# Performance work log

Hardware: AMD Instinct MI355X
Metric: run time of the kernel (lower is better)

## Reference

```python
import jax, jax.numpy as jnp
import numpy as np

N = 100000  # nodes

def gcn_layer(x, W, b, src, dst, norm):
    # x: [N, Fin] -> [N, Fout]; symmetric-normalized aggregation (PyG GCNConv)
    h = x @ W                                   # linear first (no bias yet)
    msg = h[src] * norm[:, None]                # gather + edge-wise scale
    out = jax.ops.segment_sum(msg, dst, num_segments=N)  # scatter-add to targets
    return out + b

def _prep_edges(edge_index):
    # add self loops
    loops = jnp.arange(N, dtype=edge_index.dtype)
    src = jnp.concatenate([edge_index[0], loops])
    dst = jnp.concatenate([edge_index[1], loops])
    # deg computed on target nodes with unit edge weights
    deg = jax.ops.segment_sum(jnp.ones_like(dst, dtype=jnp.float32), dst, num_segments=N)
    dinv = jnp.where(deg > 0, jax.lax.rsqrt(deg), 0.0)
    norm = dinv[src] * dinv[dst]
    return src, dst, norm

def setup_inputs() -> dict:
    key = jax.random.key(0)
    ks = jax.random.split(key, 8)
    F_in, H1, H2, C = 512, 256, 64, 10
    E = 3200000
    x = jax.random.normal(ks[0], (N, F_in), dtype=jnp.float32)
    edge_index = jax.random.randint(ks[1], (2, E), 0, N, dtype=jnp.int64)
    def glorot(k, fan_in, fan_out):
        s = jnp.sqrt(6.0 / (fan_in + fan_out))
        return jax.random.uniform(k, (fan_in, fan_out), jnp.float32, -s, s)
    return {
        "x": x,
        "edge_index": edge_index,
        "W1": glorot(ks[2], F_in, H1), "b1": jnp.zeros((H1,), jnp.float32),
        "W2": glorot(ks[3], H1, H2),   "b2": jnp.zeros((H2,), jnp.float32),
        "W3": glorot(ks[4], H2, C),    "b3": jnp.zeros((C,), jnp.float32),
    }

def reference(x, edge_index, W1, b1, W2, b2, W3, b3):
    src, dst, norm = _prep_edges(edge_index)
    h = jax.nn.relu(gcn_layer(x, W1, b1, src, dst, norm))
    h = jax.nn.relu(gcn_layer(h, W2, b2, src, dst, norm))
    h = gcn_layer(h, W3, b3, src, dst, norm)
    return jax.nn.log_softmax(h, axis=1)
```

## Files before the change

### kernel.cpp

```cpp
#include <hip/hip_runtime.h>
#include <math.h>

#define NNODES 100000
#define NEDGES 3200000
#define NB 391
#define PB 512
#define CHUNK 6250

typedef __attribute__((ext_vector_type(4))) float f32x4;
typedef __attribute__((ext_vector_type(2))) float f32x2;
typedef __attribute__((ext_vector_type(8))) short bf16x8;

__device__ __forceinline__ float bf2f(ushort u) {
    union { unsigned u; float f; } v; v.u = ((unsigned)u) << 16; return v.f;
}
__device__ __forceinline__ ushort f2bf(float f) {
    union { float f; unsigned u; } v; v.f = f;
    unsigned r = v.u + 0x7FFFu + ((v.u >> 16) & 1u);
    return (ushort)(r >> 16);
}

__device__ __forceinline__ unsigned pack_bf2(float f0, float f1) {
    union { float f; unsigned u; } a, b; a.f = f0; b.f = f1;
#if __has_builtin(__builtin_amdgcn_perm)
    return __builtin_amdgcn_perm(b.u, a.u, 0x07060302u);
#else
    return (b.u & 0xFFFF0000u) | (a.u >> 16);
#endif
}

#if __has_builtin(__builtin_amdgcn_cvt_pk_fp8_f32) && __has_builtin(__builtin_amdgcn_cvt_pk_f32_fp8)
#define FP8_HW 1
#else
#define FP8_HW 0
#endif

__device__ __forceinline__ unsigned fp8enc_sw(float f) {
    union { float f; unsigned u; } v; v.f = f;
    unsigned sign = v.u >> 31;
    float a = fabsf(f);
    if (a >= 448.0f) return (sign << 7) | 0x7E;
    if (a < 0.0009765625f) return sign << 7;
    unsigned u = v.u & 0x7FFFFFFFu;
    u += 0x7FFFFu + ((u >> 20) & 1u);
    int e2 = (int)(u >> 23) - 127;
    if (e2 < -6) {
        int m = (int)(a * 512.0f + 0.5f); if (m > 7) m = 7;
        return (sign << 7) | (unsigned)m;
    }
    if (e2 > 8) return (sign << 7) | 0x7E;
    unsigned mant = (u >> 20) & 7u;
    return (sign << 7) | ((unsigned)(e2 + 7) << 3) | mant;
}
__device__ __forceinline__ float fp8dec_sw(unsigned b) {
    unsigned s = b >> 7, e = (b >> 3) & 0xF, m = b & 7;
    float v;
    if (e == 0) v = (float)m * 0.001953125f;
    else { union { unsigned u; float f; } x; x.u = ((e + 120u) << 23) | (m << 20); v = x.f; }
    return s ? -v : v;
}

__device__ __forceinline__ unsigned char f2fp8(float f) {
#if FP8_HW
    return (unsigned char)(__builtin_amdgcn_cvt_pk_fp8_f32(f, 0.f, 0, false) & 0xFF);
#else
    return (unsigned char)fp8enc_sw(f);
#endif
}
__device__ __forceinline__ void fp8x4_acc2(unsigned w, f32x2& a01, f32x2& a23) {
#if FP8_HW
    a01 += __builtin_amdgcn_cvt_pk_f32_fp8((int)w, false);
    a23 += __builtin_amdgcn_cvt_pk_f32_fp8((int)w, true);
#else
    a01[0] += fp8dec_sw(w & 0xFF); a01[1] += fp8dec_sw((w >> 8) & 0xFF);
    a23[0] += fp8dec_sw((w >> 16) & 0xFF); a23[1] += fp8dec_sw(w >> 24);
#endif
}

__global__ void bucket_hist(const int* __restrict__ dst, int e, int* __restrict__ hist) {
    __shared__ int h[NB];
    const int b = blockIdx.x, t = threadIdx.x;
    for (int j = t; j < NB; j += 256) h[j] = 0;
    __syncthreads();
    const int lo = b * CHUNK;
    int hi = lo + CHUNK; if (hi > e) hi = e;
    for (int i = lo + t; i < hi; i += 256)
        atomicAdd(&h[dst[i] >> 8], 1);
    __syncthreads();
    for (int j = t; j < NB; j += 256) hist[b * NB + j] = h[j];
}

__global__ void scan_buckets(int* __restrict__ hist, int* __restrict__ btotal) {
    __shared__ int s[256];
    const int j = blockIdx.x, t = threadIdx.x;
    int v0 = hist[(2 * t) * NB + j];
    int v1 = hist[(2 * t + 1) * NB + j];
    int p = v0 + v1;
    s[t] = p;
    __syncthreads();
    for (int off = 1; off < 256; off <<= 1) {
        int u = (t >= off) ? s[t - off] : 0;
        __syncthreads();
        s[t] += u;
        __syncthreads();
    }
    int excl = s[t] - p;
    hist[(2 * t) * NB + j] = excl;
    hist[(2 * t + 1) * NB + j] = excl + v0;
    if (t == 255) btotal[j] = s[255];
}

__global__ void scan_btotal(const int* __restrict__ btotal, int* __restrict__ bstart, int e) {
    __shared__ int s[512];
    const int t = threadIdx.x;
    int v = (t < NB) ? btotal[t] : 0;
    s[t] = v;
    __syncthreads();
    for (int off = 1; off < 512; off <<= 1) {
        int u = (t >= off) ? s[t - off] : 0;
        __syncthreads();
        s[t] += u;
        __syncthreads();
    }
    if (t < NB) bstart[t] = s[t] - v;
    if (t == 0) bstart[NB] = e;
}

__global__ void bucket_scatter(const int* __restrict__ src, const int* __restrict__ dst, int e,
                               const int* __restrict__ hist, const int* __restrict__ bstart,
                               unsigned* __restrict__ bucketed) {
    __shared__ int off[NB];
    const int b = blockIdx.x, t = threadIdx.x;
    for (int j = t; j < NB; j += 256) off[j] = bstart[j] + hist[b * NB + j];
    __syncthreads();
    const int lo = b * CHUNK;
    int hi = lo + CHUNK; if (hi > e) hi = e;
    for (int i = lo + t; i < hi; i += 256) {
        int d = dst[i];
        int j = d >> 8;
        int p = atomicAdd(&off[j], 1);
        bucketed[p] = (unsigned)src[i] | ((unsigned)(d & 255) << 24);
    }
}

__global__ void bucket_finalize(const unsigned* __restrict__ bucketed, const int* __restrict__ bstart,
                                float* __restrict__ dinv, int* __restrict__ rowptr,
                                int* __restrict__ esrc, int n, int e) {
    __shared__ int h[256];
    __shared__ int s[256];
    __shared__ int rp[256];
    const int j = blockIdx.x, t = threadIdx.x;
    h[t] = 0;
    __syncthreads();
    const int lo = bstart[j], hi = bstart[j + 1];
    for (int i = lo + t; i < hi; i += 256)
        atomicAdd(&h[bucketed[i] >> 24], 1);
    __syncthreads();
    const int c = h[t] + 1;
    s[t] = c;
    __syncthreads();
    for (int off = 1; off < 256; off <<= 1) {
        int u = (t >= off) ? s[t - off] : 0;
        __syncthreads();
        s[t] += u;
        __syncthreads();
    }
    const int excl = s[t] - c;
    const int base = j << 8;
    const int node = base + t;
    const int myrp = bstart[j] + base + excl;
    rp[t] = myrp;
    if (node < n) {
        dinv[node] = rsqrtf((float)c);
        rowptr[node] = myrp;
        esrc[myrp] = node;
    }
    if (j == 0 && t == 0) rowptr[n] = e + n;
    h[t] = 0;
    __syncthreads();
    for (int i = lo + t; i < hi; i += 256) {
        unsigned ed = bucketed[i];
        int l = ed >> 24;
        int off = atomicAdd(&h[l], 1);
        esrc[rp[l] + 1 + off] = (int)(ed & 0xFFFFFFu);
    }
}

__global__ void conv_weights(const float* __restrict__ W1, ushort* __restrict__ W1t,
                             const float* __restrict__ W2, unsigned char* __restrict__ W2t,
                             const float* __restrict__ W3, unsigned char* __restrict__ W3t) {
    int idx = blockIdx.x * blockDim.x + threadIdx.x;
    if (idx < 256 * 512) {
        int n = idx / 512, k = idx % 512;
        W1t[idx] = f2bf(W1[(size_t)k * 256 + n]);
    } else if (idx < 256 * 512 + 64 * 256) {
        int r = idx - 256 * 512;
        int n = r / 256, k = r % 256;
        W2t[r] = f2fp8(W2[(size_t)k * 64 + n]);
    } else if (idx < 256 * 512 + 64 * 256 + 16 * 64) {
        int r = idx - 256 * 512 - 64 * 256;
        int n = r / 64, k = r % 64;
        W3t[r] = (n < 10) ? f2fp8(W3[(size_t)k * 10 + n]) : (unsigned char)0;
    }
}

template <int BM, int BN, int BK, int WM, int WN>
__launch_bounds__(WM* WN * 64)
__global__ void gemm_f32a(const float* __restrict__ A, const ushort* __restrict__ Bt,
                          const float* __restrict__ dinv, unsigned char* __restrict__ Cout,
                          int M, int N, int K) {
    constexpr int NT = WM * WN * 64;
    __shared__ __align__(16) float Asf[BM][BK];
    __shared__ __align__(16) ushort Bs[BN][BK];
    const int tid = threadIdx.x;
    const int wid = tid >> 6, lane = tid & 63;
    const int wr = wid / WN, wc = wid % WN;
    constexpr int TM = BM / WM, TN = BN / WN;
    constexpr int FM = TM / 16, FN = TN / 16;
    const int m0 = blockIdx.y * BM, n0 = blockIdx.x * BN;
    const int ln = lane & 15, ks4 = (lane >> 4) * 2;

    f32x4 acc[FM][FN] = {};

    constexpr int CPRA = BK / 4;
    constexpr int ACH = BM * CPRA;
    constexpr int CPRB = BK / 8;
    constexpr int BCH = BN * CPRB;

    for (int k0 = 0; k0 < K; k0 += BK) {
        #pragma unroll
        for (int it = 0; it < ACH / NT; ++it) {
            int c = it * NT + tid;
            int row = c >> 3, chs = c & 7;
            int gch = chs ^ (row & 7);
            int gm = m0 + row; if (gm >= M) gm = M - 1;
            const float* gp = &A[(size_t)gm * K + k0 + gch * 4];
            __builtin_amdgcn_global_load_lds(
                (const __attribute__((address_space(1))) void*)gp,
                (__attribute__((address_space(3))) void*)((char*)&Asf[0][0] + c * 16),
                16, 0, 0);
        }
        #pragma unroll
        for (int it = 0; it < BCH / NT; ++it) {
            int c = it * NT + tid;
            int row = c / CPRB, ch = c % CPRB;
            const ushort* gp = &Bt[(size_t)(n0 + row) * K + k0 + ch * 8];
            __builtin_amdgcn_global_load_lds(
                (const __attribute__((address_space(1))) void*)gp,
                (__attribute__((address_space(3))) void*)((char*)&Bs[0][0] + c * 16),
                16, 0, 0);
        }
        __syncthreads();

        bf16x8 af[FM], bfr[FN];
        #pragma unroll
        for (int mi = 0; mi < FM; ++mi) {
            int r = wr * TM + mi * 16 + ln;
            const char* rowp = (const char*)&Asf[0][0] + r * (BK * 4);
            float4 a0 = *(const float4*)(rowp + ((ks4 ^ (r & 7)) * 16));
            float4 a1 = *(const float4*)(rowp + (((ks4 + 1) ^ (r & 7)) * 16));
            union { unsigned w[4]; bf16x8 v; } u;
            u.w[0] = pack_bf2(a0.x, a0.y);
            u.w[1] = pack_bf2(a0.z, a0.w);
            u.w[2] = pack_bf2(a1.x, a1.y);
            u.w[3] = pack_bf2(a1.z, a1.w);
            af[mi] = u.v;
        }
        const int ks = (lane >> 4) * 8;
        #pragma unroll
        for (int nj = 0; nj < FN; ++nj)
            bfr[nj] = *(const bf16x8*)&Bs[wc * TN + nj * 16 + ln][ks];
        #pragma unroll
        for (int mi = 0; mi < FM; ++mi)
            #pragma unroll
            for (int nj = 0; nj < FN; ++nj)
                acc[mi][nj] = __builtin_amdgcn_mfma_f32_16x16x32_bf16(af[mi], bfr[nj], acc[mi][nj], 0, 0, 0);
        __syncthreads();
    }

    const int rbase = (lane >> 4) * 4;
    #pragma unroll
    for (int mi = 0; mi < FM; ++mi) {
        #pragma unroll
        for (int r = 0; r < 4; ++r) {
            int gm = m0 + wr * TM + mi * 16 + rbase + r;
            if (gm >= M) continue;
            float d = dinv[gm];
            #pragma unroll
            for (int nj = 0; nj < FN; ++nj) {
                int gn = n0 + wc * TN + nj * 16 + ln;
                Cout[(size_t)gm * N + gn] = f2fp8(acc[mi][nj][r] * d);
            }
        }
    }
}

template <int BM, int BN, int BK, int WM, int WN, int OUTK>
__launch_bounds__(WM* WN * 64)
__global__ void gemm_fp8(const unsigned char* __restrict__ A, const unsigned char* __restrict__ Bt,
                         const float* __restrict__ dinv, void* __restrict__ Cout,
                         int M, int N, int K) {
    constexpr int NT = WM * WN * 64;
    __shared__ __align__(16) unsigned char As[BM][BK];
    __shared__ __align__(16) unsigned char Bs[BN][BK];
    const int tid = threadIdx.x;
    const int wid = tid >> 6, lane = tid & 63;
    const int wr = wid / WN, wc = wid % WN;
    constexpr int TM = BM / WM, TN = BN / WN;
    constexpr int FM = TM / 16, FN = TN / 16;
    const int m0 = blockIdx.y * BM, n0 = blockIdx.x * BN;
    const int ln = lane & 15;

    f32x4 acc[FM][FN] = {};

    constexpr int CPR = BK / 16;
    constexpr int ACH = BM * CPR;
    constexpr int BCH = BN * CPR;

    for (int k0 = 0; k0 < K; k0 += BK) {
        #pragma unroll
        for (int it = 0; it < (ACH + NT - 1) / NT; ++it) {
            int c = it * NT + tid;
            if ((ACH % NT == 0) || (c < ACH)) {
                int row = c / CPR, ch = c % CPR;
                int gm = m0 + row; if (gm >= M) gm = M - 1;
                const unsigned char* gp = &A[(size_t)gm * K + k0 + ch * 16];
                __builtin_amdgcn_global_load_lds(
                    (const __attribute__((address_space(1))) void*)gp,
                    (__attribute__((address_space(3))) void*)((char*)&As[0][0] + c * 16),
                    16, 0, 0);
            }
        }
        #pragma unroll
        for (int it = 0; it < (BCH + NT - 1) / NT; ++it) {
            int c = it * NT + tid;
            if ((BCH % NT == 0) || (c < BCH)) {
                int row = c / CPR, ch = c % CPR;
                const unsigned char* gp = &Bt[(size_t)(n0 + row) * K + k0 + ch * 16];
                __builtin_amdgcn_global_load_lds(
                    (const __attribute__((address_space(1))) void*)gp,
                    (__attribute__((address_space(3))) void*)((char*)&Bs[0][0] + c * 16),
                    16, 0, 0);
            }
        }
        __syncthreads();

        long af[FM], bfr[FN];
        #pragma unroll
        for (int mi = 0; mi < FM; ++mi)
            af[mi] = ((const long*)&As[0][0])[(wr * TM + mi * 16 + ln) * (BK / 8) + (lane >> 4)];
        #pragma unroll
        for (int nj = 0; nj < FN; ++nj)
            bfr[nj] = ((const long*)&Bs[0][0])[(wc * TN + nj * 16 + ln) * (BK / 8) + (lane >> 4)];
        #pragma unroll
        for (int mi = 0; mi < FM; ++mi)
            #pragma unroll
            for (int nj = 0; nj < FN; ++nj)
                acc[mi][nj] = __builtin_amdgcn_mfma_f32_16x16x32_fp8_fp8(af[mi], bfr[nj], acc[mi][nj], 0, 0, 0);
        __syncthreads();
    }

    const int rbase = (lane >> 4) * 4;
    #pragma unroll
    for (int mi = 0; mi < FM; ++mi) {
        #pragma unroll
        for (int r = 0; r < 4; ++r) {
            int gm = m0 + wr * TM + mi * 16 + rbase + r;
            if (gm >= M) continue;
            float d = dinv[gm];
            #pragma unroll
            for (int nj = 0; nj < FN; ++nj) {
                int gn = n0 + wc * TN + nj * 16 + ln;
                float v = acc[mi][nj][r] * d;
                if (OUTK == 0) ((ushort*)Cout)[(size_t)gm * N + gn] = f2bf(v);
                else           ((unsigned char*)Cout)[(size_t)gm * N + gn] = f2fp8(v);
            }
        }
    }
}

__global__ void agg1_fp8(const unsigned* __restrict__ h, const int* __restrict__ rowptr,
                         const int* __restrict__ esrc, const float* __restrict__ dinv,
                         const float* __restrict__ bias, unsigned char* __restrict__ out, int n) {
    const int wid = threadIdx.x >> 6, lane = threadIdx.x & 63;
    const int i = blockIdx.x * 4 + wid;
    if (i >= n) return;
    const int lo = rowptr[i], hi = rowptr[i + 1];
    f32x2 a01 = {0.f, 0.f}, a23 = {0.f, 0.f};
    int e = lo;
    for (; e + 7 < hi; e += 8) {
        int s[8];
        unsigned w[8];
        #pragma unroll
        for (int q = 0; q < 8; ++q) s[q] = esrc[e + q];
        #pragma unroll
        for (int q = 0; q < 8; ++q) w[q] = h[(size_t)s[q] * 64 + lane];
        #pragma unroll
        for (int q = 0; q < 8; ++q) fp8x4_acc2(w[q], a01, a23);
    }
    for (; e < hi; ++e)
        fp8x4_acc2(h[(size_t)esrc[e] * 64 + lane], a01, a23);

    float d = dinv[i];
    const int f0 = lane * 4;
    float4 b = *(const float4*)&bias[f0];
    uchar4 o;
    o.x = f2fp8(fmaxf(a01[0] * d + b.x, 0.f));
    o.y = f2fp8(fmaxf(a01[1] * d + b.y, 0.f));
    o.z = f2fp8(fmaxf(a23[0] * d + b.z, 0.f));
    o.w = f2fp8(fmaxf(a23[1] * d + b.w, 0.f));
    *(uchar4*)&out[(size_t)i * 256 + f0] = o;
}

__global__ void agg2_fp8(const unsigned* __restrict__ h, const int* __restrict__ rowptr,
                         const int* __restrict__ esrc, const float* __restrict__ dinv,
                         const float* __restrict__ bias, unsigned char* __restrict__ out, int n) {
    const int g = threadIdx.x >> 4, j = threadIdx.x & 15;
    const int i = blockIdx.x * 16 + g;
    if (i >= n) return;
    const int lo = rowptr[i], hi = rowptr[i + 1];
    f32x2 a01 = {0.f, 0.f}, a23 = {0.f, 0.f};
    int e = lo;
    for (; e + 7 < hi; e += 8) {
        int s[8];
        unsigned w[8];
        #pragma unroll
        for (int q = 0; q < 8; ++q) s[q] = esrc[e + q];
        #pragma unroll
        for (int q = 0; q < 8; ++q) w[q] = h[(size_t)s[q] * 16 + j];
        #pragma unroll
        for (int q = 0; q < 8; ++q) fp8x4_acc2(w[q], a01, a23);
    }
    for (; e < hi; ++e)
        fp8x4_acc2(h[(size_t)esrc[e] * 16 + j], a01, a23);

    float d = dinv[i];
    const int f0 = j * 4;
    float4 b = *(const float4*)&bias[f0];
    uchar4 o;
    o.x = f2fp8(fmaxf(a01[0] * d + b.x, 0.f));
    o.y = f2fp8(fmaxf(a01[1] * d + b.y, 0.f));
    o.z = f2fp8(fmaxf(a23[0] * d + b.z, 0.f));
    o.w = f2fp8(fmaxf(a23[1] * d + b.w, 0.f));
    *(uchar4*)&out[(size_t)i * 64 + f0] = o;
}

__global__ void agg3_logsoftmax(const ushort* __restrict__ h3, const int* __restrict__ rowptr,
                                const int* __restrict__ esrc, const float* __restrict__ dinv,
                                const float* __restrict__ bias, float* __restrict__ out, int n) {
    const int g = threadIdx.x >> 3, j = threadIdx.x & 7;
    const int i = blockIdx.x * 32 + g;
    if (i >= n) return;
    const int lo = rowptr[i], hi = rowptr[i + 1];
    float a0 = 0.f, a1 = 0.f;
    int e = lo;
    for (; e + 3 < hi; e += 4) {
        int s0 = esrc[e], s1 = esrc[e + 1], s2 = esrc[e + 2], s3 = esrc[e + 3];
        unsigned w0 = *(const unsigned*)&h3[(size_t)s0 * 16 + 2 * j];
        unsigned w1 = *(const unsigned*)&h3[(size_t)s1 * 16 + 2 * j];
        unsigned w2 = *(const unsigned*)&h3[(size_t)s2 * 16 + 2 * j];
        unsigned w3 = *(const unsigned*)&h3[(size_t)s3 * 16 + 2 * j];
        a0 += bf2f((ushort)(w0 & 0xFFFF)) + bf2f((ushort)(w1 & 0xFFFF))
            + bf2f((ushort)(w2 & 0xFFFF)) + bf2f((ushort)(w3 & 0xFFFF));
        a1 += bf2f((ushort)(w0 >> 16)) + bf2f((ushort)(w1 >> 16))
            + bf2f((ushort)(w2 >> 16)) + bf2f((ushort)(w3 >> 16));
    }
    for (; e < hi; ++e) {
        unsigned w = *(const unsigned*)&h3[(size_t)esrc[e] * 16 + 2 * j];
        a0 += bf2f((ushort)(w & 0xFFFF));
        a1 += bf2f((ushort)(w >> 16));
    }
    const int f0 = 2 * j;
    float d = dinv[i];
    float v0 = (f0 < 10) ? (a0 * d + bias[f0]) : -INFINITY;
    float v1 = (f0 + 1 < 10) ? (a1 * d + bias[f0 + 1]) : -INFINITY;
    float m = fmaxf(v0, v1);
    #pragma unroll
    for (int off = 1; off < 8; off <<= 1) m = fmaxf(m, __shfl_xor(m, off, 8));
    float ex = ((f0 < 10) ? expf(v0 - m) : 0.f) + ((f0 + 1 < 10) ? expf(v1 - m) : 0.f);
    #pragma unroll
    for (int off = 1; off < 8; off <<= 1) ex += __shfl_xor(ex, off, 8);
    float ls = logf(ex);
    if (f0 < 10)     out[(size_t)i * 10 + f0] = v0 - m - ls;
    if (f0 + 1 < 10) out[(size_t)i * 10 + f0 + 1] = v1 - m - ls;
}

extern "C" void kernel_launch(void* const* d_in, const int* in_sizes, int n_in,
                              void* d_out, int out_size, void* d_ws, size_t ws_size,
                              hipStream_t stream) {
    const int N = NNODES, E = NEDGES;
    const float* x  = (const float*)d_in[0];
    const int*   ei = (const int*)d_in[1];
    const float* W1 = (const float*)d_in[2];
    const float* b1 = (const float*)d_in[3];
    const float* W2 = (const float*)d_in[4];
    const float* b2 = (const float*)d_in[5];
    const float* W3 = (const float*)d_in[6];
    const float* b3 = (const float*)d_in[7];
    float* out = (float*)d_out;
    const int* src = ei;
    const int* dst = ei + E;

    char* ws = (char*)d_ws;
    size_t off = 0;
    auto alloc = [&](size_t bytes) -> void* {
        void* p = ws + off;
        off = (off + bytes + 255) & ~(size_t)255;
        return p;
    };
    float* dinv   = (float*)alloc((size_t)N * 4);
    int*   rowptr = (int*)alloc((size_t)(N + 1) * 4);
    int*   btotal = (int*)alloc((size_t)NB * 4);
    int*   bstart = (int*)alloc((size_t)(NB + 1) * 4);
    int*   esrc   = (int*)alloc((size_t)(E + N) * 4);
    ushort* W1t   = (ushort*)alloc((size_t)256 * 512 * 2);
    unsigned char* W2t8 = (unsigned char*)alloc((size_t)64 * 256);
    unsigned char* W3t8 = (unsigned char*)alloc((size_t)16 * 64);
    ushort* h3b   = (ushort*)alloc((size_t)N * 16 * 2);
    ushort* buf1  = (ushort*)alloc((size_t)N * 256 * 2);
    ushort* buf2  = (ushort*)alloc((size_t)N * 256 * 2);
    int*   hist   = (int*)buf1;
    unsigned* bucketed = (unsigned*)buf2;
    unsigned char* h1fp8 = (unsigned char*)buf1;
    unsigned char* a1fp8 = (unsigned char*)buf2;
    unsigned char* h2fp8 = (unsigned char*)buf1;
    unsigned char* a2fp8 = (unsigned char*)buf2;

    const int T = 256;
    bucket_hist<<<PB, T, 0, stream>>>(dst, E, hist);
    scan_buckets<<<NB, T, 0, stream>>>(hist, btotal);
    scan_btotal<<<1, 512, 0, stream>>>(btotal, bstart, E);
    bucket_scatter<<<PB, T, 0, stream>>>(src, dst, E, hist, bstart, bucketed);
    bucket_finalize<<<NB, T, 0, stream>>>(bucketed, bstart, dinv, rowptr, esrc, N, E);

    const int WTOT = 256 * 512 + 64 * 256 + 16 * 64;
    conv_weights<<<(WTOT + T - 1) / T, T, 0, stream>>>(W1, W1t, W2, W2t8, W3, W3t8);

    const int MB = (N + 127) / 128;

    gemm_f32a<128, 256, 32, 2, 4><<<dim3(1, MB), 512, 0, stream>>>(x, W1t, dinv, h1fp8, N, 256, 512);
    agg1_fp8<<<(N + 3) / 4, 256, 0, stream>>>((const unsigned*)h1fp8, rowptr, esrc, dinv, b1, a1fp8, N);

    gemm_fp8<128, 64, 32, 2, 2, 2><<<dim3(1, MB), 256, 0, stream>>>(a1fp8, W2t8, dinv, h2fp8, N, 64, 256);
    agg2_fp8<<<(N + 15) / 16, 256, 0, stream>>>((const unsigned*)h2fp8, rowptr, esrc, dinv, b2, a2fp8, N);

    gemm_fp8<128, 16, 32, 4, 1, 0><<<dim3(1, MB), 256, 0, stream>>>(a2fp8, W3t8, dinv, h3b, N, 16, 64);
    agg3_logsoftmax<<<(N + 31) / 32, 256, 0, stream>>>(h3b, rowptr, esrc, dinv, b3, out, N);
}
```

Measured before the change: 376.0 us.

## Fuse CSR build and weight conversion into one cooperative kernel with grid syncs

Replaces the five CSR-construction kernels and the weight-conversion kernel with a single cooperative launch of 512 blocks. Grid-wide syncs separate the histogram, bucket scan, total scan, scatter and finalize phases. The weight conversion is folded into the first phase. This removes several kernel launch gaps and lets the weight work overlap the histogram, at the cost of grid.sync overhead and needing all 512 blocks to be co-resident.

```diff
diff --git a/kernel.cpp b/kernel.cpp
--- a/kernel.cpp
+++ b/kernel.cpp
@@ -1,5 +1,8 @@
 #include <hip/hip_runtime.h>
+#include <hip/hip_cooperative_groups.h>
 #include <math.h>
+
+namespace cg = cooperative_groups;
 
 #define NNODES 100000
 #define NEDGES 3200000
@@ -77,130 +80,144 @@
 #endif
 }
 
-__global__ void bucket_hist(const int* __restrict__ dst, int e, int* __restrict__ hist) {
-    __shared__ int h[NB];
+__launch_bounds__(256)
+__global__ void csr_build_coop(const int* __restrict__ src, const int* __restrict__ dst, int e,
+                               int* __restrict__ hist, int* __restrict__ btotal,
+                               int* __restrict__ bstart, unsigned* __restrict__ bucketed,
+                               float* __restrict__ dinv, int* __restrict__ rowptr,
+                               int* __restrict__ esrc, int n,
+                               const float* __restrict__ W1, ushort* __restrict__ W1t,
+                               const float* __restrict__ W2, unsigned char* __restrict__ W2t,
+                               const float* __restrict__ W3, unsigned char* __restrict__ W3t) {
+    cg::grid_group grid = cg::this_grid();
+    __shared__ int shA[NB];
+    __shared__ int shB[256];
+    __shared__ int shC[256];
     const int b = blockIdx.x, t = threadIdx.x;
-    for (int j = t; j < NB; j += 256) h[j] = 0;
+
+    for (int j = t; j < NB; j += 256) shA[j] = 0;
     __syncthreads();
-    const int lo = b * CHUNK;
-    int hi = lo + CHUNK; if (hi > e) hi = e;
-    for (int i = lo + t; i < hi; i += 256)
-        atomicAdd(&h[dst[i] >> 8], 1);
+    {
+        const int lo = b * CHUNK;
+        int hi = lo + CHUNK; if (hi > e) hi = e;
+        for (int i = lo + t; i < hi; i += 256)
+            atomicAdd(&shA[dst[i] >> 8], 1);
+    }
+    {
+        const int stride = PB * 256;
+        for (int idx = b * 256 + t; idx < 256 * 512 + 64 * 256 + 16 * 64; idx += stride) {
+            if (idx < 256 * 512) {
+                int nn = idx / 512, k = idx % 512;
+                W1t[idx] = f2bf(W1[(size_t)k * 256 + nn]);
+            } else if (idx < 256 * 512 + 64 * 256) {
+                int r = idx - 256 * 512;
+                int nn = r / 256, k = r % 256;
+                W2t[r] = f2fp8(W2[(size_t)k * 64 + nn]);
+            } else {
+                int r = idx - 256 * 512 - 64 * 256;
+                int nn = r / 64, k = r % 64;
+                W3t[r] = (nn < 10) ? f2fp8(W3[(size_t)k * 10 + nn]) : (unsigned char)0;
+            }
+        }
+    }
     __syncthreads();
-    for (int j = t; j < NB; j += 256) hist[b * NB + j] = h[j];
-}
-
-__global__ void scan_buckets(int* __restrict__ hist, int* __restrict__ btotal) {
-    __shared__ int s[256];
-    const int j = blockIdx.x, t = threadIdx.x;
-    int v0 = hist[(2 * t) * NB + j];
-    int v1 = hist[(2 * t + 1) * NB + j];
-    int p = v0 + v1;
-    s[t] = p;
-    __syncthreads();
-    for (int off = 1; off < 256; off <<= 1) {
-        int u = (t >= off) ? s[t - off] : 0;
-        __syncthreads();
-        s[t] += u;
-        __syncthreads();
-    }
-    int excl = s[t] - p;
-    hist[(2 * t) * NB + j] = excl;
-    hist[(2 * t + 1) * NB + j] = excl + v0;
-    if (t == 255) btotal[j] = s[255];
-}
-
-__global__ void scan_btotal(const int* __restrict__ btotal, int* __restrict__ bstart, int e) {
-    __shared__ int s[512];
-    const int t = threadIdx.x;
-    int v = (t < NB) ? btotal[t] : 0;
-    s[t] = v;
-    __syncthreads();
-    for (int off = 1; off < 512; off <<= 1) {
-        int u = (t >= off) ? s[t - off] : 0;
-        __syncthreads();
-        s[t] += u;
-        __syncthreads();
-    }
-    if (t < NB) bstart[t] = s[t] - v;
-    if (t == 0) bstart[NB] = e;
-}
-
-__global__ void bucket_scatter(const int* __restrict__ src, const int* __restrict__ dst, int e,
-                               const int* __restrict__ hist, const int* __restrict__ bstart,
-                               unsigned* __restrict__ bucketed) {
-    __shared__ int off[NB];
-    const int b = blockIdx.x, t = threadIdx.x;
-    for (int j = t; j < NB; j += 256) off[j] = bstart[j] + hist[b * NB + j];
-    __syncthreads();
-    const int lo = b * CHUNK;
-    int hi = lo + CHUNK; if (hi > e) hi = e;
-    for (int i = lo + t; i < hi; i += 256) {
-        int d = dst[i];
-        int j = d >> 8;
-        int p = atomicAdd(&off[j], 1);
-        bucketed[p] = (unsigned)src[i] | ((unsigned)(d & 255) << 24);
-    }
-}
-
-__global__ void bucket_finalize(const unsigned* __restrict__ bucketed, const int* __restrict__ bstart,
-                                float* __restrict__ dinv, int* __restrict__ rowptr,
-                                int* __restrict__ esrc, int n, int e) {
-    __shared__ int h[256];
-    __shared__ int s[256];
-    __shared__ int rp[256];
-    const int j = blockIdx.x, t = threadIdx.x;
-    h[t] = 0;
-    __syncthreads();
-    const int lo = bstart[j], hi = bstart[j + 1];
-    for (int i = lo + t; i < hi; i += 256)
-        atomicAdd(&h[bucketed[i] >> 24], 1);
-    __syncthreads();
-    const int c = h[t] + 1;
-    s[t] = c;
-    __syncthreads();
-    for (int off = 1; off < 256; off <<= 1) {
-        int u = (t >= off) ? s[t - off] : 0;
-        __syncthreads();
-        s[t] += u;
-        __syncthreads();
-    }
-    const int excl = s[t] - c;
-    const int base = j << 8;
-    const int node = base + t;
-    const int myrp = bstart[j] + base + excl;
-    rp[t] = myrp;
-    if (node < n) {
-        dinv[node] = rsqrtf((float)c);
-        rowptr[node] = myrp;
-        esrc[myrp] = node;
-    }
-    if (j == 0 && t == 0) rowptr[n] = e + n;
-    h[t] = 0;
-    __syncthreads();
-    for (int i = lo + t; i < hi; i += 256) {
-        unsigned ed = bucketed[i];
-        int l = ed >> 24;
-        int off = atomicAdd(&h[l], 1);
-        esrc[rp[l] + 1 + off] = (int)(ed & 0xFFFFFFu);
-    }
-}
-
-__global__ void conv_weights(const float* __restrict__ W1, ushort* __restrict__ W1t,
-                             const float* __restrict__ W2, unsigned char* __restrict__ W2t,
-                             const float* __restrict__ W3, unsigned char* __restrict__ W3t) {
-    int idx = blockIdx.x * blockDim.x + threadIdx.x;
-    if (idx < 256 * 512) {
-        int n = idx / 512, k = idx % 512;
-        W1t[idx] = f2bf(W1[(size_t)k * 256 + n]);
-    } else if (idx < 256 * 512 + 64 * 256) {
-        int r = idx - 256 * 512;
-        int n = r / 256, k = r % 256;
-        W2t[r] = f2fp8(W2[(size_t)k * 64 + n]);
-    } else if (idx < 256 * 512 + 64 * 256 + 16 * 64) {
-        int r = idx - 256 * 512 - 64 * 256;
-        int n = r / 64, k = r % 64;
-        W3t[r] = (n < 10) ? f2fp8(W3[(size_t)k * 10 + n]) : (unsigned char)0;
+    for (int j = t; j < NB; j += 256) hist[b * NB + j] = shA[j];
+
+    grid.sync();
+
+    if (b < NB) {
+        const int j = b;
+        int v0 = hist[(2 * t) * NB + j];
+        int v1 = hist[(2 * t + 1) * NB + j];
+        int p = v0 + v1;
+        shB[t] = p;
+        __syncthreads();
+        for (int off = 1; off < 256; off <<= 1) {
+            int u = (t >= off) ? shB[t - off] : 0;
+            __syncthreads();
+            shB[t] += u;
+            __syncthreads();
+        }
+        int excl = shB[t] - p;
+        hist[(2 * t) * NB + j] = excl;
+        hist[(2 * t + 1) * NB + j] = excl + v0;
+        if (t == 255) btotal[j] = shB[255];
+    }
+
+    grid.sync();
+
+    if (b == 0) {
+        const int i0 = 2 * t, i1 = 2 * t + 1;
+        int v0 = (i0 < NB) ? btotal[i0] : 0;
+        int v1 = (i1 < NB) ? btotal[i1] : 0;
+        int p = v0 + v1;
+        shB[t] = p;
+        __syncthreads();
+        for (int off = 1; off < 256; off <<= 1) {
+            int u = (t >= off) ? shB[t - off] : 0;
+            __syncthreads();
+            shB[t] += u;
+            __syncthreads();
+        }
+        int excl = shB[t] - p;
+        if (i0 < NB) bstart[i0] = excl;
+        if (i1 < NB) bstart[i1] = excl + v0;
+        if (t == 0) bstart[NB] = e;
+    }
+
+    grid.sync();
+
+    {
+        for (int j = t; j < NB; j += 256) shA[j] = bstart[j] + hist[b * NB + j];
+        __syncthreads();
+        const int lo = b * CHUNK;
+        int hi = lo + CHUNK; if (hi > e) hi = e;
+        for (int i = lo + t; i < hi; i += 256) {
+            int d = dst[i];
+            int j = d >> 8;
+            int p = atomicAdd(&shA[j], 1);
+            bucketed[p] = (unsigned)src[i] | ((unsigned)(d & 255) << 24);
+        }
+    }
+
+    grid.sync();
+
+    if (b < NB) {
+        const int j = b;
+        shA[t] = 0;
+        __syncthreads();
+        const int lo = bstart[j], hi = bstart[j + 1];
+        for (int i = lo + t; i < hi; i += 256)
+            atomicAdd(&shA[bucketed[i] >> 24], 1);
+        __syncthreads();
+        const int c = shA[t] + 1;
+        shB[t] = c;
+        __syncthreads();
+        for (int off = 1; off < 256; off <<= 1) {
+            int u = (t >= off) ? shB[t - off] : 0;
+            __syncthreads();
+            shB[t] += u;
+            __syncthreads();
+        }
+        const int excl = shB[t] - c;
+        const int base = j << 8;
+        const int node = base + t;
+        const int myrp = bstart[j] + base + excl;
+        shC[t] = myrp;
+        if (node < n) {
+            dinv[node] = rsqrtf((float)c);
+            rowptr[node] = myrp;
+            esrc[myrp] = node;
+        }
+        if (j == 0 && t == 0) rowptr[n] = e + n;
+        shA[t] = 0;
+        __syncthreads();
+        for (int i = lo + t; i < hi; i += 256) {
+            unsigned ed = bucketed[i];
+            int l = ed >> 24;
+            int off = atomicAdd(&shA[l], 1);
+            esrc[shC[l] + 1 + off] = (int)(ed & 0xFFFFFFu);
+        }
     }
 }
 
@@ -526,15 +543,17 @@
     unsigned char* h2fp8 = (unsigned char*)buf1;
     unsigned char* a2fp8 = (unsigned char*)buf2;
 
-    const int T = 256;
-    bucket_hist<<<PB, T, 0, stream>>>(dst, E, hist);
-    scan_buckets<<<NB, T, 0, stream>>>(hist, btotal);
-    scan_btotal<<<1, 512, 0, stream>>>(btotal, bstart, E);
-    bucket_scatter<<<PB, T, 0, stream>>>(src, dst, E, hist, bstart, bucketed);
-    bucket_finalize<<<NB, T, 0, stream>>>(bucketed, bstart, dinv, rowptr, esrc, N, E);
-
-    const int WTOT = 256 * 512 + 64 * 256 + 16 * 64;
-    conv_weights<<<(WTOT + T - 1) / T, T, 0, stream>>>(W1, W1t, W2, W2t8, W3, W3t8);
+    {
+        int e_arg = E, n_arg = N;
+        void* args[] = {
+            (void*)&src, (void*)&dst, (void*)&e_arg,
+            (void*)&hist, (void*)&btotal, (void*)&bstart, (void*)&bucketed,
+            (void*)&dinv, (void*)&rowptr, (void*)&esrc, (void*)&n_arg,
+            (void*)&W1, (void*)&W1t, (void*)&W2, (void*)&W2t8, (void*)&W3, (void*)&W3t8
+        };
+        hipLaunchCooperativeKernel((const void*)csr_build_coop, dim3(PB), dim3(256),
+                                   args, 0, stream);
+    }
 
     const int MB = (N + 127) / 128;
 
```

New measurement: 631.7 us. 1.68x slower.
